# Kernel optimization log

Hardware: AMD Instinct MI355X
Metric: run time of the kernel (lower is better)

Reference implementation:

```python
import jax, jax.numpy as jnp
import numpy as np

TEMPERATURE = 0.07
EPS = 1e-12  # F.normalize eps


def setup_inputs() -> dict:
    key = jax.random.key(0)
    k1, k2, k3 = jax.random.split(key, 3)
    B, D, N_CLASSES = 4096, 256, 1000
    return {
        "z_i": jax.random.normal(k1, (B, D), dtype=jnp.float32),
        "z_j": jax.random.normal(k2, (B, D), dtype=jnp.float32),
        "labels": jax.random.randint(k3, (B,), 0, N_CLASSES, dtype=jnp.int64),
    }


def _l2_normalize(x):
    norm = jnp.sqrt(jnp.sum(x * x, axis=1, keepdims=True))
    return x / jnp.maximum(norm, EPS)


def reference(z_i, z_j, labels):
    zi = _l2_normalize(z_i)
    zj = _l2_normalize(z_j)
    z = jnp.concatenate([zi, zj], axis=0)          # (2B, D)
    lab = jnp.concatenate([labels, labels], axis=0)  # (2B,)
    N = z.shape[0]

    sim = jnp.matmul(z, z.T) / TEMPERATURE          # (2B, 2B)

    eye = jnp.eye(N, dtype=bool)
    same = lab[:, None] == lab[None, :]
    pos_mask = same & ~eye                          # positives: same label, not self
    neg_mask = ~same                                # negatives: different label

    # pos_sim_i = sum of similarities over positives (a sum, per original code)
    pos_sim = jnp.sum(jnp.where(pos_mask, sim, 0.0), axis=1)  # (2B,)
    # log(neg_sim_i) = logsumexp over negatives (stable, same math as sum of exp)
    lse_neg = jax.nn.logsumexp(jnp.where(neg_mask, sim, -jnp.inf), axis=1)
    # -log(exp(p) / (exp(p) + n)) = log(1 + exp(log n - p))
    loss_i = jnp.logaddexp(0.0, lse_neg - pos_sim)  # (2B,)

    has_pos = jnp.any(pos_mask, axis=1)
    loss = jnp.sum(jnp.where(has_pos, loss_i, 0.0)) / N
    return loss
```

## Files before the change

kernel.cpp:

```cpp
#include <hip/hip_runtime.h>

#define NROWS 8192
#define BQ    4096
#define DDIM  256
#define INV_T (1.0f/0.07f)
#define K2EXP (1.4426950408889634f/0.07f)

typedef short bf16x8 __attribute__((ext_vector_type(8)));
typedef float f32x4  __attribute__((ext_vector_type(4)));
typedef unsigned short u16;

__device__ __forceinline__ u16 f2bf(float f) {
  unsigned u = __float_as_uint(f);
  u += 0x7fffu + ((u >> 16) & 1u);
  return (u16)(u >> 16);
}

__global__ void norm_cast_kernel(const float* __restrict__ zi,
                                 const float* __restrict__ zj,
                                 u16* __restrict__ zb) {
  int wave = threadIdx.x >> 6;
  int lane = threadIdx.x & 63;
  int row  = blockIdx.x * 4 + wave;
  const float* src = (row < BQ) ? (zi + (size_t)row * DDIM)
                                : (zj + (size_t)(row - BQ) * DDIM);
  float4 v = ((const float4*)src)[lane];
  float s = v.x*v.x + v.y*v.y + v.z*v.z + v.w*v.w;
  #pragma unroll
  for (int m = 32; m; m >>= 1) s += __shfl_xor(s, m, 64);
  float scale = 1.0f / fmaxf(sqrtf(s), 1e-12f);
  ushort4 o;
  o.x = f2bf(v.x * scale); o.y = f2bf(v.y * scale);
  o.z = f2bf(v.z * scale); o.w = f2bf(v.w * scale);
  ((ushort4*)(zb + (size_t)row * DDIM))[lane] = o;
}

#define GL2LDS(gp, lp) \
  __builtin_amdgcn_global_load_lds((__attribute__((address_space(1))) void*)(gp), \
                                   (__attribute__((address_space(3))) void*)(lp), 16, 0, 0)

__global__ __launch_bounds__(256) void simloss_kernel(
    const u16* __restrict__ zb, const int* __restrict__ labels,
    float* __restrict__ pos_p, float* __restrict__ neg_p) {
  __shared__ __align__(16) u16 lsA[128 * 32];
  __shared__ __align__(16) u16 lsB[128 * 32];

  const int tid  = threadIdx.x;
  const int w    = tid >> 6;
  const int lane = tid & 63;
  const int ln   = lane & 15;
  const int qd   = lane >> 4;
  const int wr   = w >> 1;
  const int wc   = w & 1;
  const int r0   = blockIdx.x * 128;
  const int cb   = blockIdx.y * 1024;

  const int strow = lane >> 2;
  const int slot  = lane & 3;
  const int stk   = (slot ^ ((strow >> 1) & 3)) * 8;
  const int rdsw  = (ln >> 1) & 3;

  int rowidx[16], rowlab[16];
  #pragma unroll
  for (int ri = 0; ri < 4; ++ri)
    #pragma unroll
    for (int r = 0; r < 4; ++r) {
      int slt = ri * 4 + r;
      int row = r0 + wr * 64 + ri * 16 + qd * 4 + r;
      rowidx[slt] = row;
      rowlab[slt] = labels[row & (BQ - 1)];
    }

  float posA[16], negA[16];
  #pragma unroll
  for (int i = 0; i < 16; ++i) { posA[i] = 0.0f; negA[i] = 0.0f; }

  for (int ci = 0; ci < 8; ++ci) {
    const int c0 = cb + ci * 128;
    int colv[4], clab[4];
    #pragma unroll
    for (int mi = 0; mi < 4; ++mi) {
      colv[mi] = c0 + wc * 64 + mi * 16 + ln;
      clab[mi] = labels[colv[mi] & (BQ - 1)];
    }

    const f32x4 z4 = {0.f, 0.f, 0.f, 0.f};
    f32x4 acc[4][4];
    #pragma unroll
    for (int ri = 0; ri < 4; ++ri)
      #pragma unroll
      for (int mi = 0; mi < 4; ++mi) acc[ri][mi] = z4;

    for (int kk = 0; kk < 8; ++kk) {
      const int k0 = kk * 32;
      #pragma unroll
      for (int j = 0; j < 2; ++j) {
        int rbase = w * 32 + j * 16;
        const u16* ga = zb + (size_t)(r0 + rbase + strow) * DDIM + k0 + stk;
        GL2LDS(ga, &lsA[rbase * 32]);
        const u16* gb = zb + (size_t)(c0 + rbase + strow) * DDIM + k0 + stk;
        GL2LDS(gb, &lsB[rbase * 32]);
      }
      __syncthreads();

      bf16x8 av[4], bv[4];
      #pragma unroll
      for (int ri = 0; ri < 4; ++ri)
        av[ri] = *(const bf16x8*)&lsA[(wr * 64 + ri * 16 + ln) * 32 + (qd ^ rdsw) * 8];
      #pragma unroll
      for (int mi = 0; mi < 4; ++mi)
        bv[mi] = *(const bf16x8*)&lsB[(wc * 64 + mi * 16 + ln) * 32 + (qd ^ rdsw) * 8];
      #pragma unroll
      for (int ri = 0; ri < 4; ++ri)
        #pragma unroll
        for (int mi = 0; mi < 4; ++mi)
          acc[ri][mi] = __builtin_amdgcn_mfma_f32_16x16x32_bf16(
              av[ri], bv[mi], acc[ri][mi], 0, 0, 0);
      __syncthreads();
    }

    #pragma unroll
    for (int ri = 0; ri < 4; ++ri)
      #pragma unroll
      for (int mi = 0; mi < 4; ++mi) {
        f32x4 v = acc[ri][mi];
        #pragma unroll
        for (int r = 0; r < 4; ++r) {
          int slt = ri * 4 + r;
          float s = v[r];
          bool same = (rowlab[slt] == clab[mi]);
          bool diag = (rowidx[slt] == colv[mi]);
          posA[slt] += (same && !diag) ? s : 0.0f;
          negA[slt] += same ? 0.0f : __builtin_amdgcn_exp2f(s * K2EXP);
        }
      }
  }

  #pragma unroll
  for (int i = 0; i < 16; ++i) {
    #pragma unroll
    for (int m = 1; m < 16; m <<= 1) {
      posA[i] += __shfl_xor(posA[i], m, 64);
      negA[i] += __shfl_xor(negA[i], m, 64);
    }
  }
  if (ln == 0) {
    int s = blockIdx.y * 2 + wc;
    #pragma unroll
    for (int i = 0; i < 16; ++i) {
      pos_p[(size_t)s * NROWS + rowidx[i]] = posA[i];
      neg_p[(size_t)s * NROWS + rowidx[i]] = negA[i];
    }
  }
}

__global__ void loss_kernel(const float* __restrict__ pos_p,
                            const float* __restrict__ neg_p,
                            float* __restrict__ out) {
  int row = blockIdx.x * 256 + threadIdx.x;
  float p = 0.0f, n = 0.0f;
  #pragma unroll
  for (int s = 0; s < 16; ++s) {
    p += pos_p[(size_t)s * NROWS + row];
    n += neg_p[(size_t)s * NROWS + row];
  }
  float l = log1pf(expf(logf(n) - p * INV_T));
  #pragma unroll
  for (int m = 32; m; m >>= 1) l += __shfl_xor(l, m, 64);
  __shared__ float red[4];
  if ((threadIdx.x & 63) == 0) red[threadIdx.x >> 6] = l;
  __syncthreads();
  if (threadIdx.x == 0) {
    float tot = red[0] + red[1] + red[2] + red[3];
    atomicAdd(out, tot * (1.0f / NROWS));
  }
}

extern "C" void kernel_launch(void* const* d_in, const int* in_sizes, int n_in,
                              void* d_out, int out_size, void* d_ws, size_t ws_size,
                              hipStream_t stream) {
  const float* zi     = (const float*)d_in[0];
  const float* zj     = (const float*)d_in[1];
  const int*   labels = (const int*)d_in[2];
  float*       out    = (float*)d_out;

  char* w = (char*)d_ws;
  u16*   zb    = (u16*)w;
  float* pos_p = (float*)(w + (size_t)NROWS * DDIM * sizeof(u16));
  float* neg_p = pos_p + 16 * NROWS;

  hipMemsetAsync(out, 0, sizeof(float), stream);
  hipLaunchKernelGGL(norm_cast_kernel, dim3(2048), dim3(256), 0, stream, zi, zj, zb);
  hipLaunchKernelGGL(simloss_kernel, dim3(64, 8), dim3(256), 0, stream,
                     zb, labels, pos_p, neg_p);
  hipLaunchKernelGGL(loss_kernel, dim3(32), dim3(256), 0, stream,
                     pos_p, neg_p, out);
}
```

Measured before the change: 121.6 us.

## Keep full A row block resident in LDS and stream B operands from global into registers

The kernel now loads the block's entire 128x256 bf16 A tile into LDS once, using an XOR swizzle, instead of reloading 32-wide K slices for every column chunk. The B operands are read straight from global memory into registers, with a one-step prefetch across the K loop. This removes the per-K-step __syncthreads and the repeated A traffic. The costs are 64KB of LDS per block, which limits occupancy, and uncoalesced per-lane 16-byte global loads for B that rely on the cache, since neighbouring waves reread the same B rows.

```diff
diff --git a/kernel.cpp b/kernel.cpp
--- a/kernel.cpp
+++ b/kernel.cpp
@@ -42,8 +42,7 @@
 __global__ __launch_bounds__(256) void simloss_kernel(
     const u16* __restrict__ zb, const int* __restrict__ labels,
     float* __restrict__ pos_p, float* __restrict__ neg_p) {
-  __shared__ __align__(16) u16 lsA[128 * 32];
-  __shared__ __align__(16) u16 lsB[128 * 32];
+  __shared__ __align__(16) u16 lsA[128 * 256];
 
   const int tid  = threadIdx.x;
   const int w    = tid >> 6;
@@ -55,10 +54,17 @@
   const int r0   = blockIdx.x * 128;
   const int cb   = blockIdx.y * 1024;
 
-  const int strow = lane >> 2;
-  const int slot  = lane & 3;
-  const int stk   = (slot ^ ((strow >> 1) & 3)) * 8;
-  const int rdsw  = (ln >> 1) & 3;
+  {
+    int rsub = lane >> 5;
+    int P    = lane & 31;
+    #pragma unroll
+    for (int i = 0; i < 16; ++i) {
+      int R = w * 32 + 2 * i + rsub;
+      int C = P ^ (R & 7);
+      const u16* g = zb + (size_t)(r0 + R) * DDIM + C * 8;
+      GL2LDS(g, &lsA[(w * 32 + 2 * i) * 256]);
+    }
+  }
 
   int rowidx[16], rowlab[16];
   #pragma unroll
@@ -75,13 +81,17 @@
   #pragma unroll
   for (int i = 0; i < 16; ++i) { posA[i] = 0.0f; negA[i] = 0.0f; }
 
+  __syncthreads();
+
   for (int ci = 0; ci < 8; ++ci) {
     const int c0 = cb + ci * 128;
     int colv[4], clab[4];
+    const u16* bbase[4];
     #pragma unroll
     for (int mi = 0; mi < 4; ++mi) {
       colv[mi] = c0 + wc * 64 + mi * 16 + ln;
       clab[mi] = labels[colv[mi] & (BQ - 1)];
+      bbase[mi] = zb + (size_t)colv[mi] * DDIM + qd * 8;
     }
 
     const f32x4 z4 = {0.f, 0.f, 0.f, 0.f};
@@ -91,32 +101,30 @@
       #pragma unroll
       for (int mi = 0; mi < 4; ++mi) acc[ri][mi] = z4;
 
+    bf16x8 bvC[4], bvN[4];
+    #pragma unroll
+    for (int mi = 0; mi < 4; ++mi) bvC[mi] = *(const bf16x8*)(bbase[mi]);
+
     for (int kk = 0; kk < 8; ++kk) {
-      const int k0 = kk * 32;
-      #pragma unroll
-      for (int j = 0; j < 2; ++j) {
-        int rbase = w * 32 + j * 16;
-        const u16* ga = zb + (size_t)(r0 + rbase + strow) * DDIM + k0 + stk;
-        GL2LDS(ga, &lsA[rbase * 32]);
-        const u16* gb = zb + (size_t)(c0 + rbase + strow) * DDIM + k0 + stk;
-        GL2LDS(gb, &lsB[rbase * 32]);
+      if (kk < 7) {
+        #pragma unroll
+        for (int mi = 0; mi < 4; ++mi)
+          bvN[mi] = *(const bf16x8*)(bbase[mi] + (kk + 1) * 32);
       }
-      __syncthreads();
-
-      bf16x8 av[4], bv[4];
-      #pragma unroll
-      for (int ri = 0; ri < 4; ++ri)
-        av[ri] = *(const bf16x8*)&lsA[(wr * 64 + ri * 16 + ln) * 32 + (qd ^ rdsw) * 8];
-      #pragma unroll
-      for (int mi = 0; mi < 4; ++mi)
-        bv[mi] = *(const bf16x8*)&lsB[(wc * 64 + mi * 16 + ln) * 32 + (qd ^ rdsw) * 8];
+      bf16x8 av[4];
+      #pragma unroll
+      for (int ri = 0; ri < 4; ++ri) {
+        int R = wr * 64 + ri * 16 + ln;
+        av[ri] = *(const bf16x8*)&lsA[R * 256 + (((kk * 4 + qd) ^ (ln & 7)) * 8)];
+      }
       #pragma unroll
       for (int ri = 0; ri < 4; ++ri)
         #pragma unroll
         for (int mi = 0; mi < 4; ++mi)
           acc[ri][mi] = __builtin_amdgcn_mfma_f32_16x16x32_bf16(
-              av[ri], bv[mi], acc[ri][mi], 0, 0, 0);
-      __syncthreads();
+              av[ri], bvC[mi], acc[ri][mi], 0, 0, 0);
+      #pragma unroll
+      for (int mi = 0; mi < 4; ++mi) bvC[mi] = bvN[mi];
     }
 
     #pragma unroll
```

Result: slower. 143.4 us (+17.9%).
